# Performance work log

Hardware: AMD Instinct MI355X
Metric: run time of the kernel (lower is better)

## Reference

```python
import jax, jax.numpy as jnp
import numpy as np


def setup_inputs() -> dict:
    key = jax.random.key(0)
    k1, k2, k3, k4, k5 = jax.random.split(key, 5)
    B, H, W, C, F = 8, 64, 64, 256, 64
    # glorot_uniform for 1x1 conv kernels [1,1,Cin,Cout]
    def glorot(k, cin, cout):
        lim = float(np.sqrt(6.0 / (cin + cout)))
        return jax.random.uniform(k, (1, 1, cin, cout), jnp.float32, -lim, lim)
    x = jax.random.normal(k1, (B, H, W, C), dtype=jnp.float32)
    Wf = glorot(k2, C, F)
    Wg = glorot(k3, C, F)
    Wh = glorot(k4, C, C)
    Wv = glorot(k5, C, C)
    gamma = jnp.zeros((1,), dtype=jnp.float32) + 0.1  # nonzero so attention path matters
    return {"x": x, "Wf": Wf, "Wg": Wg, "Wh": Wh, "Wv": Wv, "gamma": gamma}


def reference(x, Wf, Wg, Wh, Wv, gamma):
    B, H, W, C = x.shape
    N = H * W
    # 1x1 convs are pointwise matmuls over channels
    f = jnp.einsum('bhwc,cf->bhwf', x, Wf[0, 0])   # [B,H,W,F]
    g = jnp.einsum('bhwc,cf->bhwf', x, Wg[0, 0])   # [B,H,W,F]
    h = jnp.einsum('bhwc,cd->bhwd', x, Wh[0, 0])   # [B,H,W,C]
    ff = f.reshape(B, N, -1)                        # [B,N,F]
    gf = g.reshape(B, N, -1)                        # [B,N,F]
    hf = h.reshape(B, N, C)                         # [B,N,C]
    # s[b,i,j] = ff[b,i,:] . gf[b,j,:]  (no 1/sqrt(d) scaling, as in source)
    s = jnp.einsum('bif,bjf->bij', ff, gf)          # [B,N,N]
    beta = jax.nn.softmax(s, axis=-1)
    o = jnp.einsum('bij,bjc->bic', beta, hf)        # [B,N,C]
    o = o.reshape(B, H, W, C)
    o = jnp.einsum('bhwc,cd->bhwd', o, Wv[0, 0])
    return gamma * o + x
```

## Files before the change

### kernel.cpp

```cpp
#include <hip/hip_runtime.h>

typedef _Float16 half8   __attribute__((ext_vector_type(8)));
typedef _Float16 half4_t __attribute__((ext_vector_type(4)));
typedef float    float4_t __attribute__((ext_vector_type(4)));

#define B_   8
#define N_   4096
#define C_   256
#define F_   64

#if defined(__has_builtin) && __has_builtin(__builtin_amdgcn_exp2f)
#define EXP2(x) __builtin_amdgcn_exp2f(x)
#else
#define EXP2(x) exp2f(x)
#endif
#define LOG2E 1.44269504f

static __device__ __forceinline__ float4_t mfma16(half8 a, half8 b, float4_t c) {
  return __builtin_amdgcn_mfma_f32_16x16x32_f16(a, b, c, 0, 0, 0);
}

template <int CTRL>
static __device__ __forceinline__ float dpp_f(float x) {
  return __int_as_float(__builtin_amdgcn_update_dpp(
      __float_as_int(x), __float_as_int(x), CTRL, 0xF, 0xF, false));
}
static __device__ __forceinline__ float row_max16(float v) {
  v = fmaxf(v, dpp_f<0x128>(v));
  v = fmaxf(v, dpp_f<0x124>(v));
  v = fmaxf(v, dpp_f<0x122>(v));
  v = fmaxf(v, dpp_f<0x121>(v));
  return v;
}
static __device__ __forceinline__ float row_sum16(float v) {
  v += dpp_f<0x128>(v);
  v += dpp_f<0x124>(v);
  v += dpp_f<0x122>(v);
  v += dpp_f<0x121>(v);
  return v;
}

__global__ __launch_bounds__(256) void prep_whvt(const float* __restrict__ Wh,
                                                 const float* __restrict__ Wv,
                                                 _Float16* __restrict__ whvt) {
  int d = blockIdx.x;
  int c = threadIdx.x;
  const float4_t* whr = (const float4_t*)(Wh + (size_t)c * 256);
  float acc = 0.f;
#pragma unroll 8
  for (int e4 = 0; e4 < 64; ++e4) {
    float4_t w4 = whr[e4];
    acc += w4[0] * Wv[(e4 * 4 + 0) * 256 + d];
    acc += w4[1] * Wv[(e4 * 4 + 1) * 256 + d];
    acc += w4[2] * Wv[(e4 * 4 + 2) * 256 + d];
    acc += w4[3] * Wv[(e4 * 4 + 3) * 256 + d];
  }
  whvt[d * 256 + c] = (_Float16)acc;
}

__global__ __launch_bounds__(256) void prep_wfgt(const float* __restrict__ Wf,
                                                 const float* __restrict__ Wg,
                                                 _Float16* __restrict__ wfgt) {
  int n = blockIdx.x;
  int c = threadIdx.x;
  float v = (n < 64) ? Wf[c * 64 + n] : Wg[c * 64 + (n - 64)];
  wfgt[n * 256 + c] = (_Float16)v;
}

__global__ __launch_bounds__(256) void transpose_x(const float* __restrict__ x,
                                                   _Float16* __restrict__ xT) {
  __shared__ float tile[32][33];
  int b  = blockIdx.x >> 7;
  int n0 = (blockIdx.x & 127) << 5;
  int c0 = blockIdx.y << 5;
  int tid = threadIdx.x;
  int r  = tid >> 3;
  int cc = (tid & 7) << 2;
  const float* src = x + ((size_t)(b * N_ + n0 + r)) * C_ + c0 + cc;
  float4_t v = *(const float4_t*)src;
  tile[r][cc + 0] = v[0]; tile[r][cc + 1] = v[1];
  tile[r][cc + 2] = v[2]; tile[r][cc + 3] = v[3];
  __syncthreads();
  half4_t o;
  o[0] = (_Float16)tile[cc + 0][r];
  o[1] = (_Float16)tile[cc + 1][r];
  o[2] = (_Float16)tile[cc + 2][r];
  o[3] = (_Float16)tile[cc + 3][r];
  _Float16* dst = xT + ((size_t)(b * C_ + c0 + r)) * N_ + n0 + cc;
  *(half4_t*)dst = o;
}

__global__ __launch_bounds__(256) void fg_kernel(const float* __restrict__ x,
                                                 const _Float16* __restrict__ wfgt,
                                                 _Float16* __restrict__ f,
                                                 _Float16* __restrict__ g) {
  int tid  = threadIdx.x;
  int wave = tid >> 6, lane = tid & 63;
  int n16  = lane & 15, quad = lane >> 4;
  int row  = blockIdx.x * 64 + wave * 16 + n16;
  float4_t acc[8];
#pragma unroll
  for (int t = 0; t < 8; t++) acc[t] = (float4_t){0.f, 0.f, 0.f, 0.f};
  for (int k0 = 0; k0 < 256; k0 += 32) {
    const float* xp = x + (size_t)row * C_ + k0 + quad * 8;
    float4_t x0 = *(const float4_t*)xp;
    float4_t x1 = *(const float4_t*)(xp + 4);
    half8 af;
#pragma unroll
    for (int j = 0; j < 4; j++) { af[j] = (_Float16)x0[j]; af[4 + j] = (_Float16)x1[j]; }
#pragma unroll
    for (int t = 0; t < 8; t++) {
      half8 bf = *(const half8*)(wfgt + (size_t)(t * 16 + n16) * 256 + k0 + quad * 8);
      acc[t] = mfma16(af, bf, acc[t]);
    }
  }
  int orow = blockIdx.x * 64 + wave * 16 + quad * 4;
#pragma unroll
  for (int t = 0; t < 8; t++) {
#pragma unroll
    for (int r = 0; r < 4; r++) {
      _Float16 v = (_Float16)acc[t][r];
      int col = t * 16 + n16;
      if (t < 4) f[(size_t)(orow + r) * 64 + col] = v;
      else       g[(size_t)(orow + r) * 64 + col - 64] = v;
    }
  }
}

__global__ __launch_bounds__(256, 2) void flash_kernel(const _Float16* __restrict__ f,
                                                       const _Float16* __restrict__ g,
                                                       const _Float16* __restrict__ xT,
                                                       _Float16* __restrict__ a) {
  __shared__ _Float16 ktb2[2][64 * 64];
  __shared__ _Float16 ptb2[2][64 * 64];
  __shared__ float alpha_lds[2][64];
  __shared__ float linv_lds[64];

  const int b   = blockIdx.x;
  const int i0  = blockIdx.y * 64;
  const int tid = threadIdx.x;
  const int wave = tid >> 6, lane = tid & 63;
  const int n16 = lane & 15, quad = lane >> 4;
  const int nlo = n16 & 7, nhi = n16 >> 3;

  half8 qf[2];
  {
    const _Float16* qp = f + (size_t)(b * N_ + i0 + wave * 16 + n16) * 64 + quad * 8;
    qf[0] = *(const half8*)qp;
    qf[1] = *(const half8*)(qp + 32);
  }

  float4_t o_acc[16];
#pragma unroll
  for (int t = 0; t < 16; t++) o_acc[t] = (float4_t){0.f, 0.f, 0.f, 0.f};
  float m_i[4] = {-1e30f, -1e30f, -1e30f, -1e30f};
  float l_i[4] = {0.f, 0.f, 0.f, 0.f};

  const _Float16* gbase = g + (size_t)(b * N_) * 64;
  const _Float16* xbase = xT + ((size_t)b * C_ + 64 * wave) * (size_t)N_;

  const int krow = tid >> 2;
  const int kcb  = (tid & 3) << 1;
  const int krb  = krow & 7;

  {
    const _Float16* ks = gbase + (size_t)krow * 64 + (kcb << 3);
    half8 k0 = *(const half8*)ks;
    half8 k1 = *(const half8*)(ks + 8);
    _Float16* kd = ktb2[0] + krow * 64;
    *(half8*)(kd + (((kcb    ) ^ krb) << 3)) = k0;
    *(half8*)(kd + (((kcb + 1) ^ krb) << 3)) = k1;
  }
  __syncthreads();

  for (int k = 0; k < 64; ++k) {
    const int j0  = k << 6;
    const int buf = k & 1;
    const int j0n = (j0 + 64) & (N_ - 1);

    half8 kp0, kp1;
    {
      const _Float16* ks = gbase + (size_t)(j0n + krow) * 64 + (kcb << 3);
      kp0 = *(const half8*)ks;
      kp1 = *(const half8*)(ks + 8);
    }
    half8 vfr[8];
#pragma unroll
    for (int s = 0; s < 2; s++)
#pragma unroll
      for (int ct = 0; ct < 4; ct++)
        vfr[s * 4 + ct] = *(const half8*)(xbase + (size_t)(16 * ct + n16) * N_ +
                                          j0 + 32 * s + 8 * quad);

    float4_t s_acc[4];
#pragma unroll
    for (int t = 0; t < 4; t++) s_acc[t] = (float4_t){0.f, 0.f, 0.f, 0.f};
    {
      const _Float16* ktb = ktb2[buf];
      __builtin_amdgcn_s_setprio(1);
#pragma unroll
      for (int s = 0; s < 2; s++)
#pragma unroll
        for (int t = 0; t < 4; t++) {
          half8 bf = *(const half8*)(ktb + (16 * t + n16) * 64 +
                                     (((4 * s + quad) ^ nlo) << 3));
          s_acc[t] = mfma16(qf[s], bf, s_acc[t]);
        }
      __builtin_amdgcn_s_setprio(0);
    }
#pragma unroll
    for (int t = 0; t < 4; t++) s_acc[t] *= LOG2E;

    float alpha_r[4];
#pragma unroll
    for (int r = 0; r < 4; r++) {
      float v = fmaxf(fmaxf(s_acc[0][r], s_acc[1][r]),
                      fmaxf(s_acc[2][r], s_acc[3][r]));
      v = row_max16(v);
      float mn = fmaxf(m_i[r], v);
      alpha_r[r] = EXP2(m_i[r] - mn);
      m_i[r] = mn;
    }
    _Float16* pb = ptb2[buf];
#pragma unroll
    for (int r = 0; r < 4; r++) {
      float s0 = EXP2(s_acc[0][r] - m_i[r]);
      float s1 = EXP2(s_acc[1][r] - m_i[r]);
      float s2 = EXP2(s_acc[2][r] - m_i[r]);
      float s3 = EXP2(s_acc[3][r] - m_i[r]);
      float v = row_sum16(s0 + s1 + s2 + s3);
      l_i[r] = l_i[r] * alpha_r[r] + v;
      const int row = wave * 16 + 4 * quad + r;
      const int rb  = row & 7;
      _Float16* pr = pb + row * 64 + nlo;
      pr[((nhi    ) ^ rb) << 3] = (_Float16)s0;
      pr[((nhi + 2) ^ rb) << 3] = (_Float16)s1;
      pr[((nhi + 4) ^ rb) << 3] = (_Float16)s2;
      pr[((nhi + 6) ^ rb) << 3] = (_Float16)s3;
    }
    if (n16 == 0) {
#pragma unroll
      for (int r = 0; r < 4; r++)
        alpha_lds[buf][wave * 16 + 4 * quad + r] = alpha_r[r];
    }
    {
      _Float16* kd = ktb2[buf ^ 1] + krow * 64;
      *(half8*)(kd + (((kcb    ) ^ krb) << 3)) = kp0;
      *(half8*)(kd + (((kcb + 1) ^ krb) << 3)) = kp1;
    }
    __syncthreads();

#pragma unroll
    for (int ti = 0; ti < 4; ti++)
#pragma unroll
      for (int r = 0; r < 4; r++) {
        float al = alpha_lds[buf][ti * 16 + 4 * quad + r];
#pragma unroll
        for (int ct = 0; ct < 4; ct++) o_acc[ti * 4 + ct][r] *= al;
      }

    __builtin_amdgcn_s_setprio(1);
#pragma unroll
    for (int s = 0; s < 2; s++)
#pragma unroll
      for (int ti = 0; ti < 4; ti++) {
        half8 af = *(const half8*)(pb + (16 * ti + n16) * 64 +
                                   (((4 * s + quad) ^ nlo) << 3));
#pragma unroll
        for (int ct = 0; ct < 4; ct++)
          o_acc[ti * 4 + ct] = mfma16(af, vfr[s * 4 + ct], o_acc[ti * 4 + ct]);
      }
    __builtin_amdgcn_s_setprio(0);
  }

  if (n16 == 0) {
#pragma unroll
    for (int r = 0; r < 4; r++)
      linv_lds[wave * 16 + 4 * quad + r] = 1.f / l_i[r];
  }
  __syncthreads();
#pragma unroll
  for (int ti = 0; ti < 4; ti++)
#pragma unroll
    for (int r = 0; r < 4; r++) {
      float il = linv_lds[ti * 16 + 4 * quad + r];
      size_t orow = (size_t)(b * N_ + i0 + ti * 16 + 4 * quad + r) * C_;
#pragma unroll
      for (int ct = 0; ct < 4; ct++)
        a[orow + 64 * wave + 16 * ct + n16] =
            (_Float16)(o_acc[ti * 4 + ct][r] * il);
    }
}

__global__ __launch_bounds__(256) void out_kernel(const _Float16* __restrict__ a,
                                                  const _Float16* __restrict__ whvt,
                                                  const float* __restrict__ x,
                                                  const float* __restrict__ gamma,
                                                  float* __restrict__ out) {
  int tid  = threadIdx.x;
  int wave = tid >> 6, lane = tid & 63;
  int n16  = lane & 15, quad = lane >> 4;
  int row  = blockIdx.x * 64 + wave * 16 + n16;
  float4_t acc[16];
#pragma unroll
  for (int t = 0; t < 16; t++) acc[t] = (float4_t){0.f, 0.f, 0.f, 0.f};
  for (int k0 = 0; k0 < 256; k0 += 32) {
    half8 af = *(const half8*)(a + (size_t)row * C_ + k0 + quad * 8);
#pragma unroll
    for (int t = 0; t < 16; t++) {
      half8 bf = *(const half8*)(whvt + (size_t)(t * 16 + n16) * 256 + k0 + quad * 8);
      acc[t] = mfma16(af, bf, acc[t]);
    }
  }
  float gm = gamma[0];
  int orow = blockIdx.x * 64 + wave * 16 + quad * 4;
#pragma unroll
  for (int t = 0; t < 16; t++) {
#pragma unroll
    for (int r = 0; r < 4; r++) {
      size_t idx = (size_t)(orow + r) * C_ + t * 16 + n16;
      out[idx] = gm * acc[t][r] + x[idx];
    }
  }
}

extern "C" void kernel_launch(void* const* d_in, const int* in_sizes, int n_in,
                              void* d_out, int out_size, void* d_ws, size_t ws_size,
                              hipStream_t stream) {
  const float* x     = (const float*)d_in[0];
  const float* Wf    = (const float*)d_in[1];
  const float* Wg    = (const float*)d_in[2];
  const float* Wh    = (const float*)d_in[3];
  const float* Wv    = (const float*)d_in[4];
  const float* gamma = (const float*)d_in[5];
  float* out = (float*)d_out;

  char* w = (char*)d_ws;
  _Float16* whvt = (_Float16*)(w);
  _Float16* wfgt = (_Float16*)(w + 131072);
  _Float16* fb   = (_Float16*)(w + 196608);
  _Float16* gb   = (_Float16*)(w + 196608 + 4194304);
  _Float16* xT   = (_Float16*)(w + 196608 + 2 * 4194304);
  _Float16* ab   = (_Float16*)(w + 196608 + 2 * 4194304 + 16777216);

  hipLaunchKernelGGL(prep_whvt,  dim3(256),     dim3(256), 0, stream, Wh, Wv, whvt);
  hipLaunchKernelGGL(prep_wfgt,  dim3(128),     dim3(256), 0, stream, Wf, Wg, wfgt);
  hipLaunchKernelGGL(transpose_x,dim3(1024, 8), dim3(256), 0, stream, x, xT);
  hipLaunchKernelGGL(fg_kernel,  dim3(512),     dim3(256), 0, stream, x, wfgt, fb, gb);
  hipLaunchKernelGGL(flash_kernel, dim3(8, 64), dim3(256), 0, stream, fb, gb, xT, ab);
  hipLaunchKernelGGL(out_kernel, dim3(512),     dim3(256), 0, stream, ab, whvt, x, gamma, out);
}
```

Before: 293.7 us.

## Split flash attention over key halves and merge partials in output kernel

Splits the key dimension into two halves with a third grid dimension, doubling the number of blocks from 512 to 1024 for better CU occupancy. Each half writes an unnormalized fp16 partial output plus its row max and sum, and out_kernel merges them with log-sum-exp weights before the Wh·Wv projection. It also folds the log2(e) scale into Wf, skips the accumulator rescale when no row max changed, and raises launch bounds to 4 blocks per CU. The cost is extra memory traffic for two partial outputs, register pressure from the tighter launch bound, and fp16 precision risk in the unnormalized partials.

```diff
diff --git a/kernel.cpp b/kernel.cpp
--- a/kernel.cpp
+++ b/kernel.cpp
@@ -8,6 +8,8 @@
 #define N_   4096
 #define C_   256
 #define F_   64
+#define NROW (B_ * N_)
+#define OPHALF ((size_t)NROW * C_)
 
 #if defined(__has_builtin) && __has_builtin(__builtin_amdgcn_exp2f)
 #define EXP2(x) __builtin_amdgcn_exp2f(x)
@@ -63,7 +65,7 @@
                                                  _Float16* __restrict__ wfgt) {
   int n = blockIdx.x;
   int c = threadIdx.x;
-  float v = (n < 64) ? Wf[c * 64 + n] : Wg[c * 64 + (n - 64)];
+  float v = (n < 64) ? Wf[c * 64 + n] * LOG2E : Wg[c * 64 + (n - 64)];
   wfgt[n * 256 + c] = (_Float16)v;
 }
 
@@ -127,17 +129,20 @@
   }
 }
 
-__global__ __launch_bounds__(256, 2) void flash_kernel(const _Float16* __restrict__ f,
+__global__ __launch_bounds__(256, 4) void flash_kernel(const _Float16* __restrict__ f,
                                                        const _Float16* __restrict__ g,
                                                        const _Float16* __restrict__ xT,
-                                                       _Float16* __restrict__ a) {
+                                                       _Float16* __restrict__ op,
+                                                       float* __restrict__ ml) {
   __shared__ _Float16 ktb2[2][64 * 64];
   __shared__ _Float16 ptb2[2][64 * 64];
   __shared__ float alpha_lds[2][64];
-  __shared__ float linv_lds[64];
+  __shared__ int   aflag[2][4];
 
   const int b   = blockIdx.x;
   const int i0  = blockIdx.y * 64;
+  const int jh  = blockIdx.z;
+  const int jbase = jh << 11;
   const int tid = threadIdx.x;
   const int wave = tid >> 6, lane = tid & 63;
   const int n16 = lane & 15, quad = lane >> 4;
@@ -164,7 +169,7 @@
   const int krb  = krow & 7;
 
   {
-    const _Float16* ks = gbase + (size_t)krow * 64 + (kcb << 3);
+    const _Float16* ks = gbase + (size_t)(jbase + krow) * 64 + (kcb << 3);
     half8 k0 = *(const half8*)ks;
     half8 k1 = *(const half8*)(ks + 8);
     _Float16* kd = ktb2[0] + krow * 64;
@@ -173,10 +178,10 @@
   }
   __syncthreads();
 
-  for (int k = 0; k < 64; ++k) {
-    const int j0  = k << 6;
+  for (int k = 0; k < 32; ++k) {
+    const int j0  = jbase + (k << 6);
     const int buf = k & 1;
-    const int j0n = (j0 + 64) & (N_ - 1);
+    const int j0n = jbase + (((k + 1) & 31) << 6);
 
     half8 kp0, kp1;
     {
@@ -208,8 +213,6 @@
         }
       __builtin_amdgcn_s_setprio(0);
     }
-#pragma unroll
-    for (int t = 0; t < 4; t++) s_acc[t] *= LOG2E;
 
     float alpha_r[4];
 #pragma unroll
@@ -220,6 +223,12 @@
       float mn = fmaxf(m_i[r], v);
       alpha_r[r] = EXP2(m_i[r] - mn);
       m_i[r] = mn;
+    }
+    {
+      float am = fminf(fminf(alpha_r[0], alpha_r[1]),
+                       fminf(alpha_r[2], alpha_r[3]));
+      unsigned long long bm = __ballot(am < 1.0f);
+      if (lane == 0) aflag[buf][wave] = (bm != 0ULL) ? 1 : 0;
     }
     _Float16* pb = ptb2[buf];
 #pragma unroll
@@ -251,13 +260,16 @@
     __syncthreads();
 
 #pragma unroll
-    for (int ti = 0; ti < 4; ti++)
-#pragma unroll
-      for (int r = 0; r < 4; r++) {
-        float al = alpha_lds[buf][ti * 16 + 4 * quad + r];
-#pragma unroll
-        for (int ct = 0; ct < 4; ct++) o_acc[ti * 4 + ct][r] *= al;
+    for (int ti = 0; ti < 4; ti++) {
+      if (aflag[buf][ti]) {
+#pragma unroll
+        for (int r = 0; r < 4; r++) {
+          float al = alpha_lds[buf][ti * 16 + 4 * quad + r];
+#pragma unroll
+          for (int ct = 0; ct < 4; ct++) o_acc[ti * 4 + ct][r] *= al;
+        }
       }
+    }
 
     __builtin_amdgcn_s_setprio(1);
 #pragma unroll
@@ -273,26 +285,28 @@
     __builtin_amdgcn_s_setprio(0);
   }
 
+  _Float16* ob = op + (size_t)jh * OPHALF;
+#pragma unroll
+  for (int ti = 0; ti < 4; ti++)
+#pragma unroll
+    for (int r = 0; r < 4; r++) {
+      size_t orow = (size_t)(b * N_ + i0 + ti * 16 + 4 * quad + r) * C_;
+#pragma unroll
+      for (int ct = 0; ct < 4; ct++)
+        ob[orow + 64 * wave + 16 * ct + n16] = (_Float16)o_acc[ti * 4 + ct][r];
+    }
   if (n16 == 0) {
 #pragma unroll
-    for (int r = 0; r < 4; r++)
-      linv_lds[wave * 16 + 4 * quad + r] = 1.f / l_i[r];
-  }
-  __syncthreads();
-#pragma unroll
-  for (int ti = 0; ti < 4; ti++)
-#pragma unroll
-    for (int r = 0; r < 4; r++) {
-      float il = linv_lds[ti * 16 + 4 * quad + r];
-      size_t orow = (size_t)(b * N_ + i0 + ti * 16 + 4 * quad + r) * C_;
-#pragma unroll
-      for (int ct = 0; ct < 4; ct++)
-        a[orow + 64 * wave + 16 * ct + n16] =
-            (_Float16)(o_acc[ti * 4 + ct][r] * il);
-    }
-}
-
-__global__ __launch_bounds__(256) void out_kernel(const _Float16* __restrict__ a,
+    for (int r = 0; r < 4; r++) {
+      int rowg = b * N_ + i0 + wave * 16 + 4 * quad + r;
+      ml[(size_t)(jh * 2 + 0) * NROW + rowg] = m_i[r];
+      ml[(size_t)(jh * 2 + 1) * NROW + rowg] = l_i[r];
+    }
+  }
+}
+
+__global__ __launch_bounds__(256) void out_kernel(const _Float16* __restrict__ op,
+                                                  const float* __restrict__ ml,
                                                   const _Float16* __restrict__ whvt,
                                                   const float* __restrict__ x,
                                                   const float* __restrict__ gamma,
@@ -301,11 +315,24 @@
   int wave = tid >> 6, lane = tid & 63;
   int n16  = lane & 15, quad = lane >> 4;
   int row  = blockIdx.x * 64 + wave * 16 + n16;
+  float m1 = ml[row],            l1 = ml[NROW + row];
+  float m2 = ml[2 * NROW + row], l2 = ml[3 * NROW + row];
+  float ms = fmaxf(m1, m2);
+  float u1 = EXP2(m1 - ms), u2 = EXP2(m2 - ms);
+  float inv = 1.f / (l1 * u1 + l2 * u2);
+  float c1 = u1 * inv, c2 = u2 * inv;
+  const _Float16* o1 = op + (size_t)row * C_;
+  const _Float16* o2 = o1 + OPHALF;
   float4_t acc[16];
 #pragma unroll
   for (int t = 0; t < 16; t++) acc[t] = (float4_t){0.f, 0.f, 0.f, 0.f};
   for (int k0 = 0; k0 < 256; k0 += 32) {
-    half8 af = *(const half8*)(a + (size_t)row * C_ + k0 + quad * 8);
+    half8 a1 = *(const half8*)(o1 + k0 + quad * 8);
+    half8 a2 = *(const half8*)(o2 + k0 + quad * 8);
+    half8 af;
+#pragma unroll
+    for (int j = 0; j < 8; j++)
+      af[j] = (_Float16)((float)a1[j] * c1 + (float)a2[j] * c2);
 #pragma unroll
     for (int t = 0; t < 16; t++) {
       half8 bf = *(const half8*)(whvt + (size_t)(t * 16 + n16) * 256 + k0 + quad * 8);
@@ -341,12 +368,13 @@
   _Float16* fb   = (_Float16*)(w + 196608);
   _Float16* gb   = (_Float16*)(w + 196608 + 4194304);
   _Float16* xT   = (_Float16*)(w + 196608 + 2 * 4194304);
-  _Float16* ab   = (_Float16*)(w + 196608 + 2 * 4194304 + 16777216);
+  _Float16* op   = (_Float16*)(w + 196608 + 2 * 4194304 + 16777216);
+  float*    ml   = (float*)   (w + 196608 + 2 * 4194304 + 16777216 + 33554432);
 
   hipLaunchKernelGGL(prep_whvt,  dim3(256),     dim3(256), 0, stream, Wh, Wv, whvt);
   hipLaunchKernelGGL(prep_wfgt,  dim3(128),     dim3(256), 0, stream, Wf, Wg, wfgt);
   hipLaunchKernelGGL(transpose_x,dim3(1024, 8), dim3(256), 0, stream, x, xT);
   hipLaunchKernelGGL(fg_kernel,  dim3(512),     dim3(256), 0, stream, x, wfgt, fb, gb);
-  hipLaunchKernelGGL(flash_kernel, dim3(8, 64), dim3(256), 0, stream, fb, gb, xT, ab);
-  hipLaunchKernelGGL(out_kernel, dim3(512),     dim3(256), 0, stream, ab, whvt, x, gamma, out);
-}
+  hipLaunchKernelGGL(flash_kernel, dim3(8, 64, 2), dim3(256), 0, stream, fb, gb, xT, op, ml);
+  hipLaunchKernelGGL(out_kernel, dim3(512),     dim3(256), 0, stream, op, ml, whvt, x, gamma, out);
+}
```

New measurement: 652.6 us. 2.22x slower.

## Process two key blocks per flash iteration, fold log2e into Wf, skip unneeded rescales

Applied to the files above, without the earlier changes.

Each flash-attention loop iteration now handles two 64-key blocks, so there are half as many iterations and barriers. K and P LDS buffers double to hold both blocks, and the V fragments for both blocks are loaded together. The log2(e) factor moves into the prepared Wf weights, which removes a per-score multiply. A per-wave ballot flag skips the O-accumulator rescale when no row max changed. The cost is more registers and LDS per block, which may lower occupancy below the two-blocks-per-CU target and cause spills.

```diff
diff --git a/kernel.cpp b/kernel.cpp
--- a/kernel.cpp
+++ b/kernel.cpp
@@ -63,7 +63,7 @@
                                                  _Float16* __restrict__ wfgt) {
   int n = blockIdx.x;
   int c = threadIdx.x;
-  float v = (n < 64) ? Wf[c * 64 + n] : Wg[c * 64 + (n - 64)];
+  float v = (n < 64) ? Wf[c * 64 + n] * LOG2E : Wg[c * 64 + (n - 64)];
   wfgt[n * 256 + c] = (_Float16)v;
 }
 
@@ -131,10 +131,11 @@
                                                        const _Float16* __restrict__ g,
                                                        const _Float16* __restrict__ xT,
                                                        _Float16* __restrict__ a) {
-  __shared__ _Float16 ktb2[2][64 * 64];
-  __shared__ _Float16 ptb2[2][64 * 64];
+  __shared__ _Float16 ktb[2][2][64 * 64];
+  __shared__ _Float16 ptb[2][2][64 * 64];
   __shared__ float alpha_lds[2][64];
   __shared__ float linv_lds[64];
+  __shared__ int   aflag[2][4];
 
   const int b   = blockIdx.x;
   const int i0  = blockIdx.y * 64;
@@ -163,80 +164,107 @@
   const int kcb  = (tid & 3) << 1;
   const int krb  = krow & 7;
 
-  {
-    const _Float16* ks = gbase + (size_t)krow * 64 + (kcb << 3);
+#pragma unroll
+  for (int t = 0; t < 2; t++) {
+    const _Float16* ks = gbase + (size_t)(t * 64 + krow) * 64 + (kcb << 3);
     half8 k0 = *(const half8*)ks;
     half8 k1 = *(const half8*)(ks + 8);
-    _Float16* kd = ktb2[0] + krow * 64;
+    _Float16* kd = ktb[0][t] + krow * 64;
     *(half8*)(kd + (((kcb    ) ^ krb) << 3)) = k0;
     *(half8*)(kd + (((kcb + 1) ^ krb) << 3)) = k1;
   }
   __syncthreads();
 
-  for (int k = 0; k < 64; ++k) {
-    const int j0  = k << 6;
+  for (int k = 0; k < 32; ++k) {
+    const int j0A = k << 7;
+    const int j0B = j0A + 64;
+    const int set = k & 1;
     const int buf = k & 1;
-    const int j0n = (j0 + 64) & (N_ - 1);
-
-    half8 kp0, kp1;
+    const int jn  = (j0A + 128) & (N_ - 1);
+
+    half8 kpA0, kpA1, kpB0, kpB1;
     {
-      const _Float16* ks = gbase + (size_t)(j0n + krow) * 64 + (kcb << 3);
-      kp0 = *(const half8*)ks;
-      kp1 = *(const half8*)(ks + 8);
-    }
-    half8 vfr[8];
+      const _Float16* ks = gbase + (size_t)(jn + krow) * 64 + (kcb << 3);
+      kpA0 = *(const half8*)ks;
+      kpA1 = *(const half8*)(ks + 8);
+      ks += (size_t)64 * 64;
+      kpB0 = *(const half8*)ks;
+      kpB1 = *(const half8*)(ks + 8);
+    }
+    half8 vfrA[8], vfrB[8];
 #pragma unroll
     for (int s = 0; s < 2; s++)
 #pragma unroll
-      for (int ct = 0; ct < 4; ct++)
-        vfr[s * 4 + ct] = *(const half8*)(xbase + (size_t)(16 * ct + n16) * N_ +
-                                          j0 + 32 * s + 8 * quad);
-
-    float4_t s_acc[4];
-#pragma unroll
-    for (int t = 0; t < 4; t++) s_acc[t] = (float4_t){0.f, 0.f, 0.f, 0.f};
+      for (int ct = 0; ct < 4; ct++) {
+        const _Float16* vp = xbase + (size_t)(16 * ct + n16) * N_ + 32 * s + 8 * quad;
+        vfrA[s * 4 + ct] = *(const half8*)(vp + j0A);
+        vfrB[s * 4 + ct] = *(const half8*)(vp + j0B);
+      }
+
+    float4_t sA[4], sB[4];
+#pragma unroll
+    for (int t = 0; t < 4; t++) {
+      sA[t] = (float4_t){0.f, 0.f, 0.f, 0.f};
+      sB[t] = (float4_t){0.f, 0.f, 0.f, 0.f};
+    }
     {
-      const _Float16* ktb = ktb2[buf];
+      const _Float16* kA = ktb[set][0];
+      const _Float16* kB = ktb[set][1];
       __builtin_amdgcn_s_setprio(1);
 #pragma unroll
       for (int s = 0; s < 2; s++)
 #pragma unroll
         for (int t = 0; t < 4; t++) {
-          half8 bf = *(const half8*)(ktb + (16 * t + n16) * 64 +
-                                     (((4 * s + quad) ^ nlo) << 3));
-          s_acc[t] = mfma16(qf[s], bf, s_acc[t]);
+          const int off = (16 * t + n16) * 64 + (((4 * s + quad) ^ nlo) << 3);
+          sA[t] = mfma16(qf[s], *(const half8*)(kA + off), sA[t]);
+          sB[t] = mfma16(qf[s], *(const half8*)(kB + off), sB[t]);
         }
       __builtin_amdgcn_s_setprio(0);
     }
-#pragma unroll
-    for (int t = 0; t < 4; t++) s_acc[t] *= LOG2E;
 
     float alpha_r[4];
 #pragma unroll
     for (int r = 0; r < 4; r++) {
-      float v = fmaxf(fmaxf(s_acc[0][r], s_acc[1][r]),
-                      fmaxf(s_acc[2][r], s_acc[3][r]));
+      float v = fmaxf(fmaxf(fmaxf(sA[0][r], sA[1][r]), fmaxf(sA[2][r], sA[3][r])),
+                      fmaxf(fmaxf(sB[0][r], sB[1][r]), fmaxf(sB[2][r], sB[3][r])));
       v = row_max16(v);
       float mn = fmaxf(m_i[r], v);
       alpha_r[r] = EXP2(m_i[r] - mn);
       m_i[r] = mn;
     }
-    _Float16* pb = ptb2[buf];
-#pragma unroll
-    for (int r = 0; r < 4; r++) {
-      float s0 = EXP2(s_acc[0][r] - m_i[r]);
-      float s1 = EXP2(s_acc[1][r] - m_i[r]);
-      float s2 = EXP2(s_acc[2][r] - m_i[r]);
-      float s3 = EXP2(s_acc[3][r] - m_i[r]);
-      float v = row_sum16(s0 + s1 + s2 + s3);
+    {
+      float am = fminf(fminf(alpha_r[0], alpha_r[1]),
+                       fminf(alpha_r[2], alpha_r[3]));
+      unsigned long long bm = __ballot(am < 1.0f);
+      if (lane == 0) aflag[buf][wave] = (bm != 0ULL) ? 1 : 0;
+    }
+    _Float16* pA = ptb[buf][0];
+    _Float16* pB = ptb[buf][1];
+#pragma unroll
+    for (int r = 0; r < 4; r++) {
+      float a0 = EXP2(sA[0][r] - m_i[r]);
+      float a1 = EXP2(sA[1][r] - m_i[r]);
+      float a2 = EXP2(sA[2][r] - m_i[r]);
+      float a3 = EXP2(sA[3][r] - m_i[r]);
+      float b0 = EXP2(sB[0][r] - m_i[r]);
+      float b1 = EXP2(sB[1][r] - m_i[r]);
+      float b2 = EXP2(sB[2][r] - m_i[r]);
+      float b3 = EXP2(sB[3][r] - m_i[r]);
+      float v = row_sum16((a0 + a1 + a2 + a3) + (b0 + b1 + b2 + b3));
       l_i[r] = l_i[r] * alpha_r[r] + v;
       const int row = wave * 16 + 4 * quad + r;
       const int rb  = row & 7;
-      _Float16* pr = pb + row * 64 + nlo;
-      pr[((nhi    ) ^ rb) << 3] = (_Float16)s0;
-      pr[((nhi + 2) ^ rb) << 3] = (_Float16)s1;
-      pr[((nhi + 4) ^ rb) << 3] = (_Float16)s2;
-      pr[((nhi + 6) ^ rb) << 3] = (_Float16)s3;
+      const int rbase = row * 64 + nlo;
+      _Float16* prA = pA + rbase;
+      prA[((nhi    ) ^ rb) << 3] = (_Float16)a0;
+      prA[((nhi + 2) ^ rb) << 3] = (_Float16)a1;
+      prA[((nhi + 4) ^ rb) << 3] = (_Float16)a2;
+      prA[((nhi + 6) ^ rb) << 3] = (_Float16)a3;
+      _Float16* prB = pB + rbase;
+      prB[((nhi    ) ^ rb) << 3] = (_Float16)b0;
+      prB[((nhi + 2) ^ rb) << 3] = (_Float16)b1;
+      prB[((nhi + 4) ^ rb) << 3] = (_Float16)b2;
+      prB[((nhi + 6) ^ rb) << 3] = (_Float16)b3;
     }
     if (n16 == 0) {
 #pragma unroll
@@ -244,31 +272,40 @@
         alpha_lds[buf][wave * 16 + 4 * quad + r] = alpha_r[r];
     }
     {
-      _Float16* kd = ktb2[buf ^ 1] + krow * 64;
-      *(half8*)(kd + (((kcb    ) ^ krb) << 3)) = kp0;
-      *(half8*)(kd + (((kcb + 1) ^ krb) << 3)) = kp1;
+      _Float16* kd = ktb[set ^ 1][0] + krow * 64;
+      *(half8*)(kd + (((kcb    ) ^ krb) << 3)) = kpA0;
+      *(half8*)(kd + (((kcb + 1) ^ krb) << 3)) = kpA1;
+      kd = ktb[set ^ 1][1] + krow * 64;
+      *(half8*)(kd + (((kcb    ) ^ krb) << 3)) = kpB0;
+      *(half8*)(kd + (((kcb + 1) ^ krb) << 3)) = kpB1;
     }
     __syncthreads();
 
 #pragma unroll
-    for (int ti = 0; ti < 4; ti++)
-#pragma unroll
-      for (int r = 0; r < 4; r++) {
-        float al = alpha_lds[buf][ti * 16 + 4 * quad + r];
-#pragma unroll
-        for (int ct = 0; ct < 4; ct++) o_acc[ti * 4 + ct][r] *= al;
+    for (int ti = 0; ti < 4; ti++) {
+      if (aflag[buf][ti]) {
+#pragma unroll
+        for (int r = 0; r < 4; r++) {
+          float al = alpha_lds[buf][ti * 16 + 4 * quad + r];
+#pragma unroll
+          for (int ct = 0; ct < 4; ct++) o_acc[ti * 4 + ct][r] *= al;
+        }
       }
+    }
 
     __builtin_amdgcn_s_setprio(1);
 #pragma unroll
     for (int s = 0; s < 2; s++)
 #pragma unroll
       for (int ti = 0; ti < 4; ti++) {
-        half8 af = *(const half8*)(pb + (16 * ti + n16) * 64 +
-                                   (((4 * s + quad) ^ nlo) << 3));
-#pragma unroll
-        for (int ct = 0; ct < 4; ct++)
-          o_acc[ti * 4 + ct] = mfma16(af, vfr[s * 4 + ct], o_acc[ti * 4 + ct]);
+        const int off = (16 * ti + n16) * 64 + (((4 * s + quad) ^ nlo) << 3);
+        half8 afA = *(const half8*)(pA + off);
+        half8 afB = *(const half8*)(pB + off);
+#pragma unroll
+        for (int ct = 0; ct < 4; ct++) {
+          o_acc[ti * 4 + ct] = mfma16(afA, vfrA[s * 4 + ct], o_acc[ti * 4 + ct]);
+          o_acc[ti * 4 + ct] = mfma16(afB, vfrB[s * 4 + ct], o_acc[ti * 4 + ct]);
+        }
       }
     __builtin_amdgcn_s_setprio(0);
   }
```

After: 301.6 us. +2.7%, slower.

## Fuse weight prep kernels, merge x transpose into fg projection, fold log2e into Wf

Applied to the files above, without the earlier changes.

Merges the two weight-preparation kernels into one launch and folds the x transpose into the f/g projection kernel, so x is read by a single kernel and two launches disappear. The log2(e) scale is folded into Wf at prep time, which removes a per-tile multiply from the flash softmax loop. In exchange, the fused projection kernel does serial transpose work with extra barriers per block, and pre-scaling in fp16 changes rounding slightly.

```diff
diff --git a/kernel.cpp b/kernel.cpp
--- a/kernel.cpp
+++ b/kernel.cpp
@@ -40,60 +40,39 @@
   return v;
 }
 
-__global__ __launch_bounds__(256) void prep_whvt(const float* __restrict__ Wh,
-                                                 const float* __restrict__ Wv,
-                                                 _Float16* __restrict__ whvt) {
-  int d = blockIdx.x;
+__global__ __launch_bounds__(256) void prep_kernel(const float* __restrict__ Wh,
+                                                   const float* __restrict__ Wv,
+                                                   const float* __restrict__ Wf,
+                                                   const float* __restrict__ Wg,
+                                                   _Float16* __restrict__ whvt,
+                                                   _Float16* __restrict__ wfgt) {
   int c = threadIdx.x;
-  const float4_t* whr = (const float4_t*)(Wh + (size_t)c * 256);
-  float acc = 0.f;
+  if (blockIdx.x < 256) {
+    int d = blockIdx.x;
+    const float4_t* whr = (const float4_t*)(Wh + (size_t)c * 256);
+    float acc = 0.f;
 #pragma unroll 8
-  for (int e4 = 0; e4 < 64; ++e4) {
-    float4_t w4 = whr[e4];
-    acc += w4[0] * Wv[(e4 * 4 + 0) * 256 + d];
-    acc += w4[1] * Wv[(e4 * 4 + 1) * 256 + d];
-    acc += w4[2] * Wv[(e4 * 4 + 2) * 256 + d];
-    acc += w4[3] * Wv[(e4 * 4 + 3) * 256 + d];
-  }
-  whvt[d * 256 + c] = (_Float16)acc;
-}
-
-__global__ __launch_bounds__(256) void prep_wfgt(const float* __restrict__ Wf,
-                                                 const float* __restrict__ Wg,
-                                                 _Float16* __restrict__ wfgt) {
-  int n = blockIdx.x;
-  int c = threadIdx.x;
-  float v = (n < 64) ? Wf[c * 64 + n] : Wg[c * 64 + (n - 64)];
-  wfgt[n * 256 + c] = (_Float16)v;
-}
-
-__global__ __launch_bounds__(256) void transpose_x(const float* __restrict__ x,
-                                                   _Float16* __restrict__ xT) {
+    for (int e4 = 0; e4 < 64; ++e4) {
+      float4_t w4 = whr[e4];
+      acc += w4[0] * Wv[(e4 * 4 + 0) * 256 + d];
+      acc += w4[1] * Wv[(e4 * 4 + 1) * 256 + d];
+      acc += w4[2] * Wv[(e4 * 4 + 2) * 256 + d];
+      acc += w4[3] * Wv[(e4 * 4 + 3) * 256 + d];
+    }
+    whvt[d * 256 + c] = (_Float16)acc;
+  } else {
+    int n = blockIdx.x - 256;
+    float v = (n < 64) ? Wf[c * 64 + n] * LOG2E : Wg[c * 64 + (n - 64)];
+    wfgt[n * 256 + c] = (_Float16)v;
+  }
+}
+
+__global__ __launch_bounds__(256) void fgt_kernel(const float* __restrict__ x,
+                                                  const _Float16* __restrict__ wfgt,
+                                                  _Float16* __restrict__ f,
+                                                  _Float16* __restrict__ g,
+                                                  _Float16* __restrict__ xT) {
   __shared__ float tile[32][33];
-  int b  = blockIdx.x >> 7;
-  int n0 = (blockIdx.x & 127) << 5;
-  int c0 = blockIdx.y << 5;
-  int tid = threadIdx.x;
-  int r  = tid >> 3;
-  int cc = (tid & 7) << 2;
-  const float* src = x + ((size_t)(b * N_ + n0 + r)) * C_ + c0 + cc;
-  float4_t v = *(const float4_t*)src;
-  tile[r][cc + 0] = v[0]; tile[r][cc + 1] = v[1];
-  tile[r][cc + 2] = v[2]; tile[r][cc + 3] = v[3];
-  __syncthreads();
-  half4_t o;
-  o[0] = (_Float16)tile[cc + 0][r];
-  o[1] = (_Float16)tile[cc + 1][r];
-  o[2] = (_Float16)tile[cc + 2][r];
-  o[3] = (_Float16)tile[cc + 3][r];
-  _Float16* dst = xT + ((size_t)(b * C_ + c0 + r)) * N_ + n0 + cc;
-  *(half4_t*)dst = o;
-}
-
-__global__ __launch_bounds__(256) void fg_kernel(const float* __restrict__ x,
-                                                 const _Float16* __restrict__ wfgt,
-                                                 _Float16* __restrict__ f,
-                                                 _Float16* __restrict__ g) {
   int tid  = threadIdx.x;
   int wave = tid >> 6, lane = tid & 63;
   int n16  = lane & 15, quad = lane >> 4;
@@ -124,6 +103,29 @@
       if (t < 4) f[(size_t)(orow + r) * 64 + col] = v;
       else       g[(size_t)(orow + r) * 64 + col - 64] = v;
     }
+  }
+
+  const int b   = blockIdx.x >> 6;
+  const int nb  = (blockIdx.x & 63) << 6;
+  const int tr  = tid >> 3;
+  const int tc  = (tid & 7) << 2;
+#pragma unroll 1
+  for (int s = 0; s < 16; ++s) {
+    const int n0 = nb + ((s & 1) << 5);
+    const int c0 = (s >> 1) << 5;
+    __syncthreads();
+    const float* src = x + ((size_t)(b * N_ + n0 + tr)) * C_ + c0 + tc;
+    float4_t v = *(const float4_t*)src;
+    tile[tr][tc + 0] = v[0]; tile[tr][tc + 1] = v[1];
+    tile[tr][tc + 2] = v[2]; tile[tr][tc + 3] = v[3];
+    __syncthreads();
+    half4_t o;
+    o[0] = (_Float16)tile[tc + 0][tr];
+    o[1] = (_Float16)tile[tc + 1][tr];
+    o[2] = (_Float16)tile[tc + 2][tr];
+    o[3] = (_Float16)tile[tc + 3][tr];
+    _Float16* dst = xT + ((size_t)(b * C_ + c0 + tr)) * N_ + n0 + tc;
+    *(half4_t*)dst = o;
   }
 }
 
@@ -208,8 +210,6 @@
         }
       __builtin_amdgcn_s_setprio(0);
     }
-#pragma unroll
-    for (int t = 0; t < 4; t++) s_acc[t] *= LOG2E;
 
     float alpha_r[4];
 #pragma unroll
@@ -343,10 +343,10 @@
   _Float16* xT   = (_Float16*)(w + 196608 + 2 * 4194304);
   _Float16* ab   = (_Float16*)(w + 196608 + 2 * 4194304 + 16777216);
 
-  hipLaunchKernelGGL(prep_whvt,  dim3(256),     dim3(256), 0, stream, Wh, Wv, whvt);
-  hipLaunchKernelGGL(prep_wfgt,  dim3(128),     dim3(256), 0, stream, Wf, Wg, wfgt);
-  hipLaunchKernelGGL(transpose_x,dim3(1024, 8), dim3(256), 0, stream, x, xT);
-  hipLaunchKernelGGL(fg_kernel,  dim3(512),     dim3(256), 0, stream, x, wfgt, fb, gb);
+  hipLaunchKernelGGL(prep_kernel, dim3(384),   dim3(256), 0, stream,
+                     Wh, Wv, Wf, Wg, whvt, wfgt);
+  hipLaunchKernelGGL(fgt_kernel,  dim3(512),   dim3(256), 0, stream,
+                     x, wfgt, fb, gb, xT);
   hipLaunchKernelGGL(flash_kernel, dim3(8, 64), dim3(256), 0, stream, fb, gb, xT, ab);
-  hipLaunchKernelGGL(out_kernel, dim3(512),     dim3(256), 0, stream, ab, whvt, x, gamma, out);
-}
+  hipLaunchKernelGGL(out_kernel,  dim3(512),   dim3(256), 0, stream, ab, whvt, x, gamma, out);
+}
```

Measured after the change: 286.2 us. 2.5% less time.
